# Kernel optimization log

Measured on AMD Instinct MI355X. Metric: run time of the kernel, lower is better.

## Reference

```python
import jax, jax.numpy as jnp
import numpy as np

N = 8192       # nodes
IN_F = 512     # in_features
OUT_F = 256    # out_features


def setup_inputs() -> dict:
    key = jax.random.key(0)
    k1, k2, k3, k4 = jax.random.split(key, 4)
    # xavier_uniform-like scales for params
    w_scale = 1.414 * (6.0 / (IN_F + OUT_F)) ** 0.5
    a_scale = 1.414 * (6.0 / (2 * OUT_F + 1)) ** 0.5
    x = jax.random.normal(k1, (N, IN_F), jnp.float32)
    W = jax.random.uniform(k2, (IN_F, OUT_F), jnp.float32, -w_scale, w_scale)
    a = jax.random.uniform(k3, (2 * OUT_F, 1), jnp.float32, -a_scale, a_scale)
    adj = jax.random.randint(k4, (N, N), 0, 2, jnp.int32)
    return {"x": x, "W": W, "a": a, "adj": adj}


def reference(x, W, a, adj):
    # h = x @ W : [N, OUT_F]
    h = x @ W
    f = W.shape[1]
    a1, a2 = a[:f], a[f:]          # each [OUT_F, 1]
    # Original builds a_input[i,j] = concat(h_i, h_j) then matmuls with a.
    # Equivalent decomposition: e[i,j] = h_i . a1 + h_j . a2
    e = (h @ a1) + (h @ a2).T      # [N, N]
    neg = jnp.float32(-9e15)
    attention = jnp.where(adj > 0, e, neg)   # no softmax in the original
    h_prime = attention @ h        # [N, OUT_F]
    return h_prime
```

## Files before the change

### kernel.cpp

```cpp
#include <hip/hip_runtime.h>


#define NEG_BIG (-9000000000000000.0f)
#define POS_BIG (9000000000000000.0f)

typedef __bf16 bf16x8 __attribute__((ext_vector_type(8)));
typedef float f32x16 __attribute__((ext_vector_type(16)));

static __device__ __forceinline__ unsigned short f2bf(float f) {
  unsigned u = __builtin_bit_cast(unsigned, f);
  u = u + 0x7FFFu + ((u >> 16) & 1u);
  return (unsigned short)(u >> 16);
}
static __device__ __forceinline__ float bfbits2f(unsigned hi16) {
  return __builtin_bit_cast(float, hi16 << 16);
}
static __device__ __forceinline__ unsigned pk2(float a, float b) {
  return (unsigned)f2bf(a) | ((unsigned)f2bf(b) << 16);
}
static __device__ __forceinline__ bf16x8 asbf(int4 q) {
  return __builtin_bit_cast(bf16x8, q);
}
static __device__ __forceinline__ f32x16 mfma(bf16x8 a, int4 b, f32x16 c) {
  return __builtin_amdgcn_mfma_f32_32x32x16_bf16(a, asbf(b), c, 0, 0, 0);
}
static __device__ __forceinline__ bf16x8 expand8(unsigned b) {
  union { unsigned w[4]; bf16x8 f; } r;
  r.w[0] = ((b & 1u)        | ((b & 2u)   << 15)) * 0x3F80u;
  r.w[1] = (((b >> 2) & 1u) | ((b & 8u)   << 13)) * 0x3F80u;
  r.w[2] = (((b >> 4) & 1u) | ((b & 32u)  << 11)) * 0x3F80u;
  r.w[3] = (((b >> 6) & 1u) | ((b & 128u) << 9))  * 0x3F80u;
  return r.f;
}

__global__ __launch_bounds__(256) void k0_bits(const int* __restrict__ adj,
                                               unsigned char* __restrict__ bitB) {
  const int t = threadIdx.x, rb = blockIdx.x;
  const int* base = adj + (size_t)rb * 4 * 8192 + t * 32;
  unsigned* outw = (unsigned*)(bitB + (size_t)rb * 4 * 1024 + t * 4);
#pragma unroll 2
  for (int rr = 0; rr < 4; ++rr) {
    const int4* p = (const int4*)(base + (size_t)rr * 8192);
    int4 q[8];
#pragma unroll
    for (int k = 0; k < 8; ++k) q[k] = p[k];
    unsigned word = 0;
#pragma unroll
    for (int i = 0; i < 4; ++i) {
      int4 u = q[2 * i], v = q[2 * i + 1];
      unsigned by = (u.x & 1) | ((u.y & 1) << 1) | ((u.z & 1) << 2) | ((u.w & 1) << 3)
                  | ((v.x & 1) << 4) | ((v.y & 1) << 5) | ((v.z & 1) << 6) | ((v.w & 1) << 7);
      word |= by << (8 * i);
    }
    outw[rr * 256] = word;
  }
}

__global__ void k1a_wt(const float* __restrict__ W, unsigned short* __restrict__ WT,
                       float* __restrict__ T) {
  const int i = blockIdx.x * 256 + threadIdx.x;
  const int k = i >> 8, n = i & 255;
  WT[n * 512 + k] = f2bf(W[i]);
  if (blockIdx.x == 0) T[threadIdx.x] = 0.f;
}

__global__ __launch_bounds__(256) void k1b_h(const float* __restrict__ x,
    const unsigned short* __restrict__ WT, unsigned short* __restrict__ hP) {
  __shared__ unsigned short XS[64 * 264];
  const int t = threadIdx.x;
  const int mt = blockIdx.x;
  const int m0 = mt << 5;
  const int row = t >> 3, c7 = t & 7;
  const float* xr = x + (size_t)(m0 + row) * 512 + c7 * 4;
  const int gb = c7 >> 1, off = (t & 1) * 4;
#pragma unroll
  for (int j = 0; j < 16; ++j) {
    float4 v = *(const float4*)(xr + 32 * j);
    *(uint2*)&XS[(gb + 4 * j) * 264 + row * 8 + off] =
        make_uint2(pk2(v.x, v.y), pk2(v.z, v.w));
  }
  __syncthreads();
  const int w = t >> 6, l = t & 63, l31 = l & 31, lh = l >> 5;
  f32x16 acc0, acc1;
  for (int i = 0; i < 16; ++i) { acc0[i] = 0.f; acc1[i] = 0.f; }
  const int nt0 = w * 2;
  const unsigned short* w0 = WT + (size_t)(nt0 * 32 + l31) * 512 + lh * 8;
  const unsigned short* w1 = w0 + 32 * 512;
  const char* XB = (const char*)XS + lh * 528 + l31 * 16;
#pragma unroll 4
  for (int ks = 0; ks < 32; ++ks) {
    bf16x8 Af = *(const bf16x8*)(XB + ks * 1056);
    int4 b0 = *(const int4*)(w0 + ks * 16);
    int4 b1 = *(const int4*)(w1 + ks * 16);
    acc0 = mfma(Af, b0, acc0);
    acc1 = mfma(Af, b1, acc1);
  }
#pragma unroll
  for (int reg = 0; reg < 16; ++reg) {
    const int mm = (reg & 3) + 8 * (reg >> 2) + 4 * lh;
    hP[(size_t)mt * 8192 + (nt0 * 32 + l31) * 32 + mm] = f2bf(acc0[reg]);
    hP[(size_t)mt * 8192 + ((nt0 + 1) * 32 + l31) * 32 + mm] = f2bf(acc1[reg]);
  }
}

__global__ __launch_bounds__(256) void k2_colsum(const unsigned short* __restrict__ hP,
                                                 float* __restrict__ T) {
  const int t = threadIdx.x;
  const int b = blockIdx.x;
  const int4* p = (const int4*)(hP + (size_t)b * 8192 + t * 32);
  int4 q0 = p[0], q1 = p[1], q2 = p[2], q3 = p[3];
  float s = 0.f;
  const unsigned* u0 = (const unsigned*)&q0;
  const unsigned* u1 = (const unsigned*)&q1;
  const unsigned* u2 = (const unsigned*)&q2;
  const unsigned* u3 = (const unsigned*)&q3;
#pragma unroll
  for (int i = 0; i < 4; ++i) {
    s += bfbits2f(u0[i] & 0xFFFFu) + bfbits2f(u0[i] >> 16);
    s += bfbits2f(u1[i] & 0xFFFFu) + bfbits2f(u1[i] >> 16);
    s += bfbits2f(u2[i] & 0xFFFFu) + bfbits2f(u2[i] >> 16);
    s += bfbits2f(u3[i] & 0xFFFFu) + bfbits2f(u3[i] >> 16);
  }
  atomicAdd(&T[t], s);
}

__global__ void k2b_init(const float* __restrict__ T, float* __restrict__ out) {
  const int i = blockIdx.x * 256 + threadIdx.x;
  const int n4 = (i & 63) * 4;
  float4 tv = *(const float4*)(T + n4);
  float4 o;
  o.x = NEG_BIG * tv.x; o.y = NEG_BIG * tv.y;
  o.z = NEG_BIG * tv.z; o.w = NEG_BIG * tv.w;
  ((float4*)out)[i] = o;
}

template<int MODE>
__global__ __launch_bounds__(256, 4) void k3_att(const unsigned char* __restrict__ bitB,
    const unsigned short* __restrict__ hP, float* __restrict__ outp) {
  const int t = threadIdx.x, blk = blockIdx.x;
  const int s = blk & 7;
  const int g = blk >> 3;
  const int rt = g >> 1;
  const int w = t >> 6, l = t & 63, l31 = l & 31, lh = l >> 5;
  const int nt = (g & 1) * 4 + w;
  const int R0 = rt * 64;

  const unsigned char* bp0 = bitB + (size_t)(R0 + l31) * 1024 + s * 128;
  const unsigned char* bp1 = bp0 + (size_t)32 * 1024;
  const unsigned short* hB = hP + (size_t)(s * 32) * 8192
                              + (size_t)(nt * 32 + l31) * 32 + lh * 8;
  const unsigned shl = lh * 8, shh = shl + 16;

  f32x16 acc0, acc1;
#pragma unroll
  for (int i = 0; i < 16; ++i) { acc0[i] = 0.f; acc1[i] = 0.f; }

#pragma unroll 1
  for (int gi = 0; gi < 8; ++gi) {
    int4 w0 = *(const int4*)(bp0 + gi * 16);
    int4 w1 = *(const int4*)(bp1 + gi * 16);
    const unsigned* u0 = (const unsigned*)&w0;
    const unsigned* u1 = (const unsigned*)&w1;
#pragma unroll
    for (int q = 0; q < 4; ++q) {
      const unsigned short* hb = hB + (size_t)(gi * 4 + q) * 8192;
      int4 bv0 = *(const int4*)(hb);
      int4 bv1 = *(const int4*)(hb + 16);
      const unsigned d0 = u0[q], d1 = u1[q];
      bf16x8 A00 = expand8((d0 >> shl) & 255u);
      bf16x8 A01 = expand8((d0 >> shh) & 255u);
      bf16x8 A10 = expand8((d1 >> shl) & 255u);
      bf16x8 A11 = expand8((d1 >> shh) & 255u);
      acc0 = mfma(A00, bv0, acc0);
      acc1 = mfma(A10, bv0, acc1);
      acc0 = mfma(A01, bv1, acc0);
      acc1 = mfma(A11, bv1, acc1);
    }
  }

  const int nn = nt * 32 + l31;
#pragma unroll
  for (int mt = 0; mt < 2; ++mt) {
    const f32x16& a = mt ? acc1 : acc0;
#pragma unroll
    for (int reg = 0; reg < 16; ++reg) {
      const int rr = R0 + mt * 32 + (reg & 3) + 8 * (reg >> 2) + 4 * lh;
      if (MODE == 0) {
        outp[(size_t)s * 2097152 + (size_t)rr * 256 + nn] = a[reg];
      } else {
        atomicAdd(outp + (size_t)rr * 256 + nn, POS_BIG * a[reg]);
      }
    }
  }
}

__global__ __launch_bounds__(256) void k4_reduce(const float* __restrict__ P,
    const float* __restrict__ T, float* __restrict__ out) {
  const int i = blockIdx.x * 256 + threadIdx.x;
  float4 tv = *(const float4*)(T + (i & 63) * 4);
  const float4* P4 = (const float4*)P;
  float sx = 0.f, sy = 0.f, sz = 0.f, sw = 0.f;
#pragma unroll
  for (int sp = 0; sp < 8; ++sp) {
    float4 v = P4[(size_t)sp * 524288 + i];
    sx += v.x; sy += v.y; sz += v.z; sw += v.w;
  }
  float4 o;
  o.x = POS_BIG * sx + NEG_BIG * tv.x;
  o.y = POS_BIG * sy + NEG_BIG * tv.y;
  o.z = POS_BIG * sz + NEG_BIG * tv.z;
  o.w = POS_BIG * sw + NEG_BIG * tv.w;
  ((float4*)out)[i] = o;
}

extern "C" void kernel_launch(void* const* d_in, const int* in_sizes, int n_in,
                              void* d_out, int out_size, void* d_ws, size_t ws_size,
                              hipStream_t stream) {
  const float* x = (const float*)d_in[0];
  const float* W = (const float*)d_in[1];
  const int* adj = (const int*)d_in[3];
  float* out = (float*)d_out;
  char* ws = (char*)d_ws;
  unsigned short* WT = (unsigned short*)(ws);
  unsigned short* hP = (unsigned short*)(ws + (1 << 20));
  float* T = (float*)(ws + (6 << 20));
  unsigned char* bitB = (unsigned char*)(ws + (16 << 20));
  float* P = (float*)(ws + (32 << 20));

  const bool fit = ws_size >= ((size_t)(32 << 20) + (size_t)64 * 1024 * 1024);

  k0_bits<<<2048, 256, 0, stream>>>(adj, bitB);
  k1a_wt<<<512, 256, 0, stream>>>(W, WT, T);
  k1b_h<<<256, 256, 0, stream>>>(x, WT, hP);
  k2_colsum<<<256, 256, 0, stream>>>(hP, T);
  if (fit) {
    k3_att<0><<<2048, 256, 0, stream>>>(bitB, hP, P);
    k4_reduce<<<2048, 256, 0, stream>>>(P, T, out);
  } else {
    k2b_init<<<2048, 256, 0, stream>>>(T, out);
    k3_att<1><<<2048, 256, 0, stream>>>(bitB, hP, out);
  }
}
```

Measured before the change: 473.6 us.

## Reshape attention tiling to 4-way K split with atomics and register double-buffered B loads

The attention-matmul kernel now uses 32-row tiles with a 4-way split over the neighbor dimension instead of 64-row tiles with an 8-way split. It accumulates directly into the output via atomicAdd after an init kernel, dropping the partial buffer and the separate reduce kernel. B-operand loads are double-buffered in registers so the next loads are issued before the current MFMAs, and the occupancy hint rises to 6 blocks per CU. This removes the write and reread of the 64MB partial buffer, at the cost of atomic contention and halved reuse of each loaded h tile across rows.

```diff
diff --git a/kernel.cpp b/kernel.cpp
--- a/kernel.cpp
+++ b/kernel.cpp
@@ -134,83 +134,66 @@
   ((float4*)out)[i] = o;
 }
 
-template<int MODE>
-__global__ __launch_bounds__(256, 4) void k3_att(const unsigned char* __restrict__ bitB,
-    const unsigned short* __restrict__ hP, float* __restrict__ outp) {
+__global__ __launch_bounds__(256, 6) void k3_att(const unsigned char* __restrict__ bitB,
+    const unsigned short* __restrict__ hP, float* __restrict__ out) {
   const int t = threadIdx.x, blk = blockIdx.x;
-  const int s = blk & 7;
-  const int g = blk >> 3;
-  const int rt = g >> 1;
+  const int s = blk & 3;
+  const int u = blk >> 2;
+  const int rt = u >> 1;
   const int w = t >> 6, l = t & 63, l31 = l & 31, lh = l >> 5;
-  const int nt = (g & 1) * 4 + w;
-  const int R0 = rt * 64;
-
-  const unsigned char* bp0 = bitB + (size_t)(R0 + l31) * 1024 + s * 128;
-  const unsigned char* bp1 = bp0 + (size_t)32 * 1024;
-  const unsigned short* hB = hP + (size_t)(s * 32) * 8192
+  const int nt = (u & 1) * 4 + w;
+  const int R0 = rt * 32;
+
+  const unsigned char* bq = bitB + (size_t)(R0 + l31) * 1024 + s * 256;
+  const unsigned short* hB = hP + (size_t)(s * 64) * 8192
                               + (size_t)(nt * 32 + l31) * 32 + lh * 8;
-  const unsigned shl = lh * 8, shh = shl + 16;
-
-  f32x16 acc0, acc1;
-#pragma unroll
-  for (int i = 0; i < 16; ++i) { acc0[i] = 0.f; acc1[i] = 0.f; }
+  const unsigned sh0 = lh * 8, sh1 = sh0 + 16;
+
+  f32x16 acc;
+#pragma unroll
+  for (int i = 0; i < 16; ++i) acc[i] = 0.f;
+
+  int4 Ba[4], Bb[4];
+
+#define BL(dst, Q)                                                          \
+  {                                                                         \
+    const unsigned short* hq = hB + (size_t)(Q) * 8192;                     \
+    dst[0] = *(const int4*)(hq);                                            \
+    dst[1] = *(const int4*)(hq + 16);                                       \
+    dst[2] = *(const int4*)(hq + 8192);                                     \
+    dst[3] = *(const int4*)(hq + 8192 + 16);                                \
+  }
+
+  BL(Ba, 0)
 
 #pragma unroll 1
   for (int gi = 0; gi < 8; ++gi) {
-    int4 w0 = *(const int4*)(bp0 + gi * 16);
-    int4 w1 = *(const int4*)(bp1 + gi * 16);
-    const unsigned* u0 = (const unsigned*)&w0;
-    const unsigned* u1 = (const unsigned*)&w1;
-#pragma unroll
-    for (int q = 0; q < 4; ++q) {
-      const unsigned short* hb = hB + (size_t)(gi * 4 + q) * 8192;
-      int4 bv0 = *(const int4*)(hb);
-      int4 bv1 = *(const int4*)(hb + 16);
-      const unsigned d0 = u0[q], d1 = u1[q];
-      bf16x8 A00 = expand8((d0 >> shl) & 255u);
-      bf16x8 A01 = expand8((d0 >> shh) & 255u);
-      bf16x8 A10 = expand8((d1 >> shl) & 255u);
-      bf16x8 A11 = expand8((d1 >> shh) & 255u);
-      acc0 = mfma(A00, bv0, acc0);
-      acc1 = mfma(A10, bv0, acc1);
-      acc0 = mfma(A01, bv1, acc0);
-      acc1 = mfma(A11, bv1, acc1);
+    int4 u0 = *(const int4*)(bq + gi * 32);
+    int4 u1 = *(const int4*)(bq + gi * 32 + 16);
+    const unsigned* uw0 = (const unsigned*)&u0;
+    const unsigned* uw1 = (const unsigned*)&u1;
+#pragma unroll
+    for (int qq = 0; qq < 4; ++qq) {
+      const int Q = gi * 8 + qq * 2;
+      int4* cur = (qq & 1) ? Bb : Ba;
+      int4* nxt = (qq & 1) ? Ba : Bb;
+      if (Q + 2 < 64) { BL(nxt, Q + 2) }
+      const unsigned wA = (qq < 2) ? uw0[qq * 2]     : uw1[(qq - 2) * 2];
+      const unsigned wB = (qq < 2) ? uw0[qq * 2 + 1] : uw1[(qq - 2) * 2 + 1];
+      acc = mfma(expand8((wA >> sh0) & 255u), cur[0], acc);
+      acc = mfma(expand8((wA >> sh1) & 255u), cur[1], acc);
+      acc = mfma(expand8((wB >> sh0) & 255u), cur[2], acc);
+      acc = mfma(expand8((wB >> sh1) & 255u), cur[3], acc);
     }
   }
+#undef BL
 
   const int nn = nt * 32 + l31;
 #pragma unroll
-  for (int mt = 0; mt < 2; ++mt) {
-    const f32x16& a = mt ? acc1 : acc0;
-#pragma unroll
-    for (int reg = 0; reg < 16; ++reg) {
-      const int rr = R0 + mt * 32 + (reg & 3) + 8 * (reg >> 2) + 4 * lh;
-      if (MODE == 0) {
-        outp[(size_t)s * 2097152 + (size_t)rr * 256 + nn] = a[reg];
-      } else {
-        atomicAdd(outp + (size_t)rr * 256 + nn, POS_BIG * a[reg]);
-      }
-    }
-  }
-}
-
-__global__ __launch_bounds__(256) void k4_reduce(const float* __restrict__ P,
-    const float* __restrict__ T, float* __restrict__ out) {
-  const int i = blockIdx.x * 256 + threadIdx.x;
-  float4 tv = *(const float4*)(T + (i & 63) * 4);
-  const float4* P4 = (const float4*)P;
-  float sx = 0.f, sy = 0.f, sz = 0.f, sw = 0.f;
-#pragma unroll
-  for (int sp = 0; sp < 8; ++sp) {
-    float4 v = P4[(size_t)sp * 524288 + i];
-    sx += v.x; sy += v.y; sz += v.z; sw += v.w;
-  }
-  float4 o;
-  o.x = POS_BIG * sx + NEG_BIG * tv.x;
-  o.y = POS_BIG * sy + NEG_BIG * tv.y;
-  o.z = POS_BIG * sz + NEG_BIG * tv.z;
-  o.w = POS_BIG * sw + NEG_BIG * tv.w;
-  ((float4*)out)[i] = o;
+  for (int reg = 0; reg < 16; ++reg) {
+    const int rr = R0 + (reg & 3) + 8 * (reg >> 2) + 4 * lh;
+    atomicAdd(out + (size_t)rr * 256 + nn, POS_BIG * acc[reg]);
+  }
 }
 
 extern "C" void kernel_launch(void* const* d_in, const int* in_sizes, int n_in,
@@ -225,19 +208,11 @@
   unsigned short* hP = (unsigned short*)(ws + (1 << 20));
   float* T = (float*)(ws + (6 << 20));
   unsigned char* bitB = (unsigned char*)(ws + (16 << 20));
-  float* P = (float*)(ws + (32 << 20));
-
-  const bool fit = ws_size >= ((size_t)(32 << 20) + (size_t)64 * 1024 * 1024);
 
   k0_bits<<<2048, 256, 0, stream>>>(adj, bitB);
   k1a_wt<<<512, 256, 0, stream>>>(W, WT, T);
   k1b_h<<<256, 256, 0, stream>>>(x, WT, hP);
   k2_colsum<<<256, 256, 0, stream>>>(hP, T);
-  if (fit) {
-    k3_att<0><<<2048, 256, 0, stream>>>(bitB, hP, P);
-    k4_reduce<<<2048, 256, 0, stream>>>(P, T, out);
-  } else {
-    k2b_init<<<2048, 256, 0, stream>>>(T, out);
-    k3_att<1><<<2048, 256, 0, stream>>>(bitB, hP, out);
-  }
-}
+  k2b_init<<<2048, 256, 0, stream>>>(T, out);
+  k3_att<<<2048, 256, 0, stream>>>(bitB, hP, out);
+}
```

After: 485.3 us. +2.5%, slower.
